# Kernel tuning notes

Hardware: AMD Instinct MI355X
Metric: run time of the kernel (lower is better)

The kernel has to match this reference:

```python
import jax, jax.numpy as jnp
import numpy as np

B, T, V, RNN, N_OBJ = 1024, 48, 2000, 64, 25

def _lstm_cell(x, h, c, W_ih, W_hh, b_ih, b_hh):
    # PyTorch LSTMCell: gate order i, f, g, o
    gates = x @ W_ih.T + h @ W_hh.T + b_ih + b_hh
    i, f, g, o = jnp.split(gates, 4, axis=-1)
    c2 = jax.nn.sigmoid(f) * c + jax.nn.sigmoid(i) * jnp.tanh(g)
    return jax.nn.sigmoid(o) * jnp.tanh(c2), c2

def _attend(memory, h2, w1, b1, w2, b2):
    # memory: [B, 25, 4], h2: [B, 25, RNN]
    x = jnp.concatenate([h2, memory], axis=2)            # [B, 25, RNN+4]
    s = (jax.nn.relu(x @ w1.T + b1) @ w2.T + b2)[..., 0]  # [B, 25]
    w = jax.nn.softmax(s, axis=1)
    return jnp.einsum('bn,bnd->bd', w, memory)            # [B, 4]

def setup_inputs() -> dict:
    key = jax.random.key(0)
    ks = jax.random.split(key, 32)
    f = lambda k, shape: jax.random.normal(k, shape, dtype=jnp.float32) * 0.05
    return dict(
        inst=jax.random.randint(ks[0], (B, T), 1, V + 1),
        prev_canvas=jax.random.uniform(ks[1], (B, N_OBJ, 4), dtype=jnp.float32),
        final_canvas=jax.random.uniform(ks[2], (B, N_OBJ, 4), dtype=jnp.float32),
        embed=f(ks[3], (V + 1, 64)),
        W_ih_att=f(ks[4], (4 * RNN, 128)), W_hh_att=f(ks[5], (4 * RNN, RNN)),
        b_ih_att=f(ks[6], (4 * RNN,)), b_hh_att=f(ks[7], (4 * RNN,)),
        W_ih_lang=f(ks[8], (4 * RNN, 2 * RNN)), W_hh_lang=f(ks[9], (4 * RNN, RNN)),
        b_ih_lang=f(ks[10], (4 * RNN,)), b_hh_lang=f(ks[11], (4 * RNN,)),
        fc_out_w=f(ks[12], (V + 1, RNN)), fc_out_b=f(ks[13], (V + 1,)),
        att1_w1=f(ks[14], (32, RNN + 4)), att1_b1=f(ks[15], (32,)),
        att1_w2=f(ks[16], (1, 32)), att1_b2=f(ks[17], (1,)),
        att2_w1=f(ks[18], (32, RNN + 4)), att2_b1=f(ks[19], (32,)),
        att2_w2=f(ks[20], (1, 32)), att2_b2=f(ks[21], (1,)),
        trans_w1=f(ks[22], (32, 8)), trans_b1=f(ks[23], (32,)),
        trans_w2=f(ks[24], (RNN, 32)), trans_b2=f(ks[25], (RNN,)),
    )

def reference(inst, prev_canvas, final_canvas, embed, W_ih_att, W_hh_att, b_ih_att, b_hh_att, W_ih_lang, W_hh_lang, b_ih_lang, b_hh_lang, fc_out_w, fc_out_b, att1_w1, att1_b1, att1_w2, att1_b2, att2_w1, att2_b1, att2_w2, att2_b2, trans_w1, trans_b1, trans_w2, trans_b2):
    # compute_diff_canvas
    mask = prev_canvas.sum(axis=2, keepdims=True) > 0
    diff_canvas = jnp.where(mask, -1.0, final_canvas)  # [B, 25, 4]
    batch = inst.shape[0]
    h0 = jnp.zeros((batch, RNN), dtype=jnp.float32)

    def step(carry, it):
        h_att, c_att, h_lang, c_lang = carry
        xt = embed[it]  # [B, 64]
        h_att, c_att = _lstm_cell(jnp.concatenate([h_lang, xt], axis=1), h_att, c_att, W_ih_att, W_hh_att, b_ih_att, b_hh_att)
        h2 = jnp.broadcast_to(h_att[:, None, :], (batch, N_OBJ, RNN))
        a1 = _attend(diff_canvas, h2, att1_w1, att1_b1, att1_w2, att1_b2)
        a2 = _attend(prev_canvas, h2, att2_w1, att2_b1, att2_w2, att2_b2)
        att = jnp.concatenate([a1, a2], axis=1)  # [B, 8]
        att = jax.nn.relu(att @ trans_w1.T + trans_b1) @ trans_w2.T + trans_b2  # [B, RNN]
        h_lang, c_lang = _lstm_cell(jnp.concatenate([att, h_att], axis=1), h_lang, c_lang, W_ih_lang, W_hh_lang, b_ih_lang, b_hh_lang)
        logp = jax.nn.log_softmax(h_lang @ fc_out_w.T + fc_out_b, axis=1)  # [B, V+1]
        return (h_att, c_att, h_lang, c_lang), logp

    xs = inst[:, :-1].T  # [T-1, B]; inst has no all-zero column so all steps run
    _, outs = jax.lax.scan(step, (h0, h0, h0, h0), xs)
    return jnp.transpose(outs, (1, 0, 2))  # [B, T-1, V+1]
```

## Files before the change

kernel.cpp:

```cpp
#include <hip/hip_runtime.h>

#define BATCH 1024
#define TT 48
#define NSTEP 47
#define VOC 2001
#define RNN 64
#define NOBJ 25
#define NROWS (BATCH*NSTEP)
#define NTILE 126
#define NPAD 2016

typedef _Float16 h2 __attribute__((ext_vector_type(2)));
typedef _Float16 h8 __attribute__((ext_vector_type(8)));
typedef short short8 __attribute__((ext_vector_type(8)));
typedef float f32x4 __attribute__((ext_vector_type(4)));

__device__ __forceinline__ float fdot2f(h2 a, h2 b, float c){
#if __has_builtin(__builtin_amdgcn_fdot2)
    return __builtin_amdgcn_fdot2(a, b, c, false);
#else
    return c + (float)a[0]*(float)b[0] + (float)a[1]*(float)b[1];
#endif
}

__device__ __forceinline__ float dot8(h8 w, h8 x, float acc){
    acc = fdot2f(__builtin_shufflevector(w,w,0,1), __builtin_shufflevector(x,x,0,1), acc);
    acc = fdot2f(__builtin_shufflevector(w,w,2,3), __builtin_shufflevector(x,x,2,3), acc);
    acc = fdot2f(__builtin_shufflevector(w,w,4,5), __builtin_shufflevector(x,x,4,5), acc);
    acc = fdot2f(__builtin_shufflevector(w,w,6,7), __builtin_shufflevector(x,x,6,7), acc);
    return acc;
}

__device__ __forceinline__ float sigf(float x){ return 1.f/(1.f+__expf(-x)); }
__device__ __forceinline__ float tanh_(float x){
    float e = __expf(2.f*fminf(x, 15.f));
    return (e-1.f)/(e+1.f);
}
__device__ __forceinline__ unsigned short bf16r(float f){
    unsigned u = __float_as_uint(f);
    return (unsigned short)((u + 0x7FFFu + ((u>>16)&1u)) >> 16);
}


__global__ void k_pre(const float* __restrict__ prev, const float* __restrict__ fin,
                      const float* __restrict__ a1w1, const float* __restrict__ a1b1,
                      const float* __restrict__ a2w1, const float* __restrict__ a2b1,
                      float* __restrict__ diff, float* __restrict__ pre1, float* __restrict__ pre2){
    int idx = blockIdx.x*256 + threadIdx.x;
    if (idx >= BATCH*NOBJ) return;
    float p0 = prev[idx*4+0], p1 = prev[idx*4+1], p2 = prev[idx*4+2], p3 = prev[idx*4+3];
    bool masked = (p0+p1+p2+p3) > 0.f;
    float d0 = masked ? -1.f : fin[idx*4+0];
    float d1 = masked ? -1.f : fin[idx*4+1];
    float d2 = masked ? -1.f : fin[idx*4+2];
    float d3 = masked ? -1.f : fin[idx*4+3];
    diff[idx*4+0]=d0; diff[idx*4+1]=d1; diff[idx*4+2]=d2; diff[idx*4+3]=d3;
    for (int j=0;j<32;++j){
        const float* w1 = a1w1 + j*68 + 64;
        const float* w2 = a2w1 + j*68 + 64;
        pre1[idx*32+j] = a1b1[j] + d0*w1[0] + d1*w1[1] + d2*w1[2] + d3*w1[3];
        pre2[idx*32+j] = a2b1[j] + p0*w2[0] + p1*w2[1] + p2*w2[2] + p3*w2[3];
    }
}

__global__ void k_embw(const float* __restrict__ embed, const float* __restrict__ Wia,
                       const float* __restrict__ bia, const float* __restrict__ bha,
                       float* __restrict__ embW){
    int v = blockIdx.x, g = threadIdx.x;
    __shared__ float er[64];
    if (g < 64) er[g] = embed[v*64+g];
    __syncthreads();
    float acc = bia[g] + bha[g];
    const float* wr = Wia + g*128 + 64;
    #pragma unroll 8
    for (int k=0;k<64;++k) acc += er[k]*wr[k];
    embW[v*256+g] = acc;
}

__global__ void k_packrow(const float* __restrict__ src, _Float16* __restrict__ dst,
                          int srcK, int koff, int K, int total){
    int idx = blockIdx.x*256 + threadIdx.x;
    if (idx >= total) return;
    int k = idx % K, g = idx / K;
    dst[idx] = (_Float16)src[g*srcK + koff + k];
}

__global__ void k_weff(const float* __restrict__ Wil, const float* __restrict__ tw2,
                       const float* __restrict__ tb2, const float* __restrict__ bil,
                       const float* __restrict__ bhl, _Float16* __restrict__ Weff,
                       float* __restrict__ biasL2){
    __shared__ float t2[64*32];
    int g = threadIdx.x;
    for (int i=g;i<2048;i+=256) t2[i] = tw2[i];
    __syncthreads();
    float accs[32];
    #pragma unroll
    for (int m=0;m<32;++m) accs[m]=0.f;
    float bf = bil[g] + bhl[g];
    for (int d=0;d<64;++d){
        float w = Wil[g*128 + d];
        bf += w * tb2[d];
        #pragma unroll
        for (int m=0;m<32;++m) accs[m] += w * t2[d*32+m];
    }
    #pragma unroll
    for (int m=0;m<32;++m) Weff[g*32+m] = (_Float16)accs[m];
    biasL2[g] = bf;
}

__global__ void k_fcbpad(const float* __restrict__ fcb_in, float* __restrict__ fcb){
    int i = blockIdx.x*256 + threadIdx.x;
    if (i >= NPAD) return;
    fcb[i] = (i < VOC) ? fcb_in[i] : -1e30f;
}

__global__ void k_fragb(const float* __restrict__ fcw, unsigned short* __restrict__ fragB){
    int idx = blockIdx.x*256 + threadIdx.x;
    int lane = idx & 63, kh = (idx>>6)&1, tile = idx>>7;
    int n = tile*16 + (lane & 15);
    int k = kh*32 + (lane >> 4)*8;
    unsigned short* d = fragB + (size_t)((tile*2+kh)*64 + lane)*8;
    #pragma unroll
    for (int i=0;i<8;++i)
        d[i] = (n < VOC) ? bf16r(fcw[n*64 + k + i]) : (unsigned short)0;
}


__global__ __launch_bounds__(256, 2) void k_recur(
    const int* __restrict__ inst, const float* __restrict__ embW,
    const float* __restrict__ diff, const float* __restrict__ prev,
    const float* __restrict__ pre1, const float* __restrict__ pre2,
    const _Float16* __restrict__ attLp, const _Float16* __restrict__ attHp,
    const _Float16* __restrict__ wLhap, const _Float16* __restrict__ wLhlp,
    const _Float16* __restrict__ Weffp, const float* __restrict__ biasL2,
    const _Float16* __restrict__ w1fp,
    const float* __restrict__ a1w2, const float* __restrict__ a1b2,
    const float* __restrict__ a2w2, const float* __restrict__ a2b2,
    const float* __restrict__ tw1, const float* __restrict__ tb1,
    unsigned short* __restrict__ h_hist)
{
    const int tid = threadIdx.x;
    const int rb  = blockIdx.x;

    __shared__ float gbuf[256];
    __shared__ __align__(16) _Float16 hl16[64];
    __shared__ __align__(16) _Float16 ha16[64];
    __shared__ __align__(16) _Float16 u16[32];
    __shared__ float hpart[64];
    __shared__ float sbuf[2][32];
    __shared__ float att8s[8];
    __shared__ __align__(16) float preS[2][25][36];
    __shared__ float memS[2*25*4];
    __shared__ __align__(16) _Float16 w1fS[64*72];
    __shared__ float tw1S[256], tb1S[32], w2S[2][32], b2S[2];
    __shared__ int   tokS[NSTEP];
    __shared__ float biasS[256];

    for (int i=tid;i<NSTEP;i+=256) tokS[i] = inst[rb*TT + i];
    for (int i=tid;i<1600;i+=256){
        int h = i/800, rem = i - h*800, n = rem>>5, k = rem&31;
        preS[h][n][k] = (h ? pre2 : pre1)[(size_t)(rb*NOBJ+n)*32 + k];
    }
    for (int i=tid;i<200;i+=256)
        memS[i] = (i<100 ? diff : prev)[(size_t)rb*100 + (i%100)];
    for (int i=tid;i<4096;i+=256){
        int r = i>>6, k = i&63;
        w1fS[r*72+k] = w1fp[i];
    }
    if (tid<256) tw1S[tid] = tw1[tid];
    if (tid<32)  tb1S[tid] = tb1[tid];
    if (tid<64)  w2S[tid>>5][tid&31] = (tid<32 ? a1w2 : a2w2)[tid&31];
    if (tid<2)   b2S[tid] = tid ? a2b2[0] : a1b2[0];
    biasS[tid] = biasL2[tid];
    if (tid<64){ hl16[tid]=(_Float16)0.f; ha16[tid]=(_Float16)0.f; }

    h8 wAL[8], wAH[8], wLHa[8], wLHl[8], wEf[4];
    {
        const h8* p0 = (const h8*)(attLp + (size_t)tid*64);
        const h8* p1 = (const h8*)(attHp + (size_t)tid*64);
        const h8* p2 = (const h8*)(wLhap + (size_t)tid*64);
        const h8* p3 = (const h8*)(wLhlp + (size_t)tid*64);
        const h8* p4 = (const h8*)(Weffp + (size_t)tid*32);
        #pragma unroll
        for (int k=0;k<8;++k){ wAL[k]=p0[k]; wAH[k]=p1[k]; wLHa[k]=p2[k]; wLHl[k]=p3[k]; }
        #pragma unroll
        for (int k=0;k<4;++k) wEf[k]=p4[k];
    }
    float c_att = 0.f, c_lang = 0.f;
    __syncthreads();

    const int wave = tid>>6, lane = tid&63;

    for (int t=0;t<NSTEP;++t){
        float acc = embW[(size_t)tokS[t]*256 + tid];
        {
            const h8* xh = (const h8*)hl16;
            const h8* xa = (const h8*)ha16;
            #pragma unroll
            for (int k=0;k<8;++k) acc = dot8(wAL[k], xh[k], acc);
            #pragma unroll
            for (int k=0;k<8;++k) acc = dot8(wAH[k], xa[k], acc);
        }
        gbuf[tid] = acc;
        __syncthreads();
        if (tid < 64){
            float i_=sigf(gbuf[tid]), f_=sigf(gbuf[64+tid]);
            float g_=tanh_(gbuf[128+tid]), o_=sigf(gbuf[192+tid]);
            c_att = f_*c_att + i_*g_;
            ha16[tid] = (_Float16)(o_*tanh_(c_att));
        }
        __syncthreads();

        if (wave==1){
            const h8* xa = (const h8*)ha16;
            const h8* wr = (const h8*)&w1fS[lane*72];
            float hp = 0.f;
            #pragma unroll
            for (int k=0;k<8;++k) hp = dot8(wr[k], xa[k], hp);
            hpart[lane] = hp;
        }
        __syncthreads();

        if (wave==2){
            int half = lane>>5, n = lane&31;
            if (n < NOBJ){
                const float4* pp = (const float4*)&preS[half][n][0];
                const float*  hp = &hpart[half*32];
                const float*  w2 = &w2S[half][0];
                float a = b2S[half];
                #pragma unroll
                for (int i=0;i<8;++i){
                    float4 pv = pp[i];
                    a += fmaxf(hp[4*i+0]+pv.x,0.f)*w2[4*i+0]
                       + fmaxf(hp[4*i+1]+pv.y,0.f)*w2[4*i+1]
                       + fmaxf(hp[4*i+2]+pv.z,0.f)*w2[4*i+2]
                       + fmaxf(hp[4*i+3]+pv.w,0.f)*w2[4*i+3];
                }
                sbuf[half][n] = a;
            }
        }
        __syncthreads();

        if (tid>=192 && tid<200){
            int j = tid-192, half = j>>2, d = j&3;
            const float* ss = &sbuf[half][0];
            const float* mem = &memS[half*100];
            float m = -1e30f;
            for (int n=0;n<NOBJ;++n) m = fmaxf(m, ss[n]);
            float s=0.f, a=0.f;
            for (int n=0;n<NOBJ;++n){ float e=__expf(ss[n]-m); s+=e; a+=e*mem[n*4+d]; }
            att8s[j] = a/s;
        }
        __syncthreads();

        if (tid < 32){
            float u = tb1S[tid];
            #pragma unroll
            for (int i=0;i<8;++i) u += att8s[i]*tw1S[tid*8+i];
            u16[tid] = (_Float16)fmaxf(u, 0.f);
        }
        __syncthreads();

        float acc2 = biasS[tid];
        {
            const h8* xu = (const h8*)u16;
            const h8* xa = (const h8*)ha16;
            const h8* xh = (const h8*)hl16;
            #pragma unroll
            for (int k=0;k<4;++k) acc2 = dot8(wEf[k], xu[k], acc2);
            #pragma unroll
            for (int k=0;k<8;++k) acc2 = dot8(wLHa[k], xa[k], acc2);
            #pragma unroll
            for (int k=0;k<8;++k) acc2 = dot8(wLHl[k], xh[k], acc2);
        }
        gbuf[tid] = acc2;
        __syncthreads();
        if (tid < 64){
            float i_=sigf(gbuf[tid]), f_=sigf(gbuf[64+tid]);
            float g_=tanh_(gbuf[128+tid]), o_=sigf(gbuf[192+tid]);
            c_lang = f_*c_lang + i_*g_;
            float hL = o_*tanh_(c_lang);
            hl16[tid] = (_Float16)hL;
            h_hist[((size_t)rb*NSTEP + t)*64 + tid] = bf16r(hL);
        }
        __syncthreads();
    }
}


__global__ __launch_bounds__(256) void k_fc(const unsigned short* __restrict__ h_hist,
                                            const unsigned short* __restrict__ fragB,
                                            const float* __restrict__ fcb,
                                            float* __restrict__ out)
{
    const int tid = threadIdx.x;
    const int w = tid >> 6, lane = tid & 63;
    const int q = lane >> 4, l16 = lane & 15;
    const int rowbase = blockIdx.x*16;

    const short8 a0 = *(const short8*)(h_hist + (size_t)(rowbase + l16)*64 + q*8);
    const short8 a1 = *(const short8*)(h_hist + (size_t)(rowbase + l16)*64 + 32 + q*8);

    float m[4], s[4];
    #pragma unroll
    for (int i=0;i<4;++i){ m[i] = -INFINITY; s[i] = 0.f; }

    for (int tile = w; tile < NTILE; tile += 4){
        const short8 b0 = *(const short8*)(fragB + (size_t)((tile*2+0)*64 + lane)*8);
        const short8 b1 = *(const short8*)(fragB + (size_t)((tile*2+1)*64 + lane)*8);
        f32x4 acc = {0.f,0.f,0.f,0.f};
        acc = __builtin_amdgcn_mfma_f32_16x16x32_bf16(a0, b0, acc, 0, 0, 0);
        acc = __builtin_amdgcn_mfma_f32_16x16x32_bf16(a1, b1, acc, 0, 0, 0);
        float bias = fcb[tile*16 + l16];
        #pragma unroll
        for (int i=0;i<4;++i){
            float v = acc[i] + bias;
            float nm = fmaxf(m[i], v);
            s[i] = s[i]*__expf(m[i]-nm) + __expf(v-nm);
            m[i] = nm;
        }
    }
    #pragma unroll
    for (int i=0;i<4;++i){
        #pragma unroll
        for (int off=1; off<16; off<<=1){
            float om = __shfl_xor(m[i], off, 64);
            float os = __shfl_xor(s[i], off, 64);
            float nm = fmaxf(m[i], om);
            s[i] = s[i]*__expf(m[i]-nm) + os*__expf(om-nm);
            m[i] = nm;
        }
    }
    __shared__ float lm[4][16], ls[4][16], fm[16], fl[16];
    if (l16 == 0){
        #pragma unroll
        for (int i=0;i<4;++i){ lm[w][q*4+i] = m[i]; ls[w][q*4+i] = s[i]; }
    }
    __syncthreads();
    if (tid < 16){
        float M = -INFINITY, S = 0.f;
        #pragma unroll
        for (int ww=0;ww<4;++ww){
            float om = lm[ww][tid], os = ls[ww][tid];
            float nm = fmaxf(M, om);
            S = S*__expf(M-nm) + os*__expf(om-nm);
            M = nm;
        }
        fm[tid] = M; fl[tid] = __logf(S);
    }
    __syncthreads();
    float Mr[4], Lr[4];
    #pragma unroll
    for (int i=0;i<4;++i){ Mr[i] = fm[q*4+i]; Lr[i] = fl[q*4+i]; }

    for (int tile = w; tile < NTILE; tile += 4){
        const short8 b0 = *(const short8*)(fragB + (size_t)((tile*2+0)*64 + lane)*8);
        const short8 b1 = *(const short8*)(fragB + (size_t)((tile*2+1)*64 + lane)*8);
        f32x4 acc = {0.f,0.f,0.f,0.f};
        acc = __builtin_amdgcn_mfma_f32_16x16x32_bf16(a0, b0, acc, 0, 0, 0);
        acc = __builtin_amdgcn_mfma_f32_16x16x32_bf16(a1, b1, acc, 0, 0, 0);
        int col = tile*16 + l16;
        if (col < VOC){
            float bias = fcb[col];
            #pragma unroll
            for (int i=0;i<4;++i)
                out[(size_t)(rowbase + q*4 + i)*VOC + col] = acc[i] + bias - Mr[i] - Lr[i];
        }
    }
}


extern "C" void kernel_launch(void* const* d_in, const int* in_sizes, int n_in,
                              void* d_out, int out_size, void* d_ws, size_t ws_size,
                              hipStream_t stream)
{
    const int*   inst  = (const int*)  d_in[0];
    const float* prev  = (const float*)d_in[1];
    const float* fin   = (const float*)d_in[2];
    const float* embed = (const float*)d_in[3];
    const float* Wia   = (const float*)d_in[4];
    const float* Wha   = (const float*)d_in[5];
    const float* bia   = (const float*)d_in[6];
    const float* bha   = (const float*)d_in[7];
    const float* Wil   = (const float*)d_in[8];
    const float* Whl   = (const float*)d_in[9];
    const float* bil   = (const float*)d_in[10];
    const float* bhl   = (const float*)d_in[11];
    const float* fcw   = (const float*)d_in[12];
    const float* fcbi  = (const float*)d_in[13];
    const float* a1w1  = (const float*)d_in[14];
    const float* a1b1  = (const float*)d_in[15];
    const float* a1w2  = (const float*)d_in[16];
    const float* a1b2  = (const float*)d_in[17];
    const float* a2w1  = (const float*)d_in[18];
    const float* a2b1  = (const float*)d_in[19];
    const float* a2w2  = (const float*)d_in[20];
    const float* a2b2  = (const float*)d_in[21];
    const float* tw1   = (const float*)d_in[22];
    const float* tb1   = (const float*)d_in[23];
    const float* tw2   = (const float*)d_in[24];
    const float* tb2   = (const float*)d_in[25];
    float* out = (float*)d_out;

    char* wsb = (char*)d_ws; size_t off = 0;
    auto alloc = [&](size_t bytes)->char*{
        char* p = wsb + off; off = (off + bytes + 511) & ~(size_t)511; return p;
    };
    float*          embW  = (float*)alloc((size_t)VOC*256*4);
    float*          diff  = (float*)alloc((size_t)BATCH*NOBJ*4*4);
    float*          pre1  = (float*)alloc((size_t)BATCH*NOBJ*32*4);
    float*          pre2  = (float*)alloc((size_t)BATCH*NOBJ*32*4);
    _Float16*       attLp = (_Float16*)alloc((size_t)256*64*2);
    _Float16*       attHp = (_Float16*)alloc((size_t)256*64*2);
    _Float16*       wLhap = (_Float16*)alloc((size_t)256*64*2);
    _Float16*       wLhlp = (_Float16*)alloc((size_t)256*64*2);
    _Float16*       Weffp = (_Float16*)alloc((size_t)256*32*2);
    _Float16*       w1fp  = (_Float16*)alloc((size_t)64*64*2);
    float*          biasL2= (float*)alloc(256*4);
    float*          fcb   = (float*)alloc((size_t)NPAD*4);
    unsigned short* hhist = (unsigned short*)alloc((size_t)NROWS*64*2);
    unsigned short* fragB = (unsigned short*)alloc((size_t)NTILE*2*64*8*2);

    k_pre    <<<(BATCH*NOBJ+255)/256, 256, 0, stream>>>(prev, fin, a1w1, a1b1, a2w1, a2b1, diff, pre1, pre2);
    k_embw   <<<VOC, 256, 0, stream>>>(embed, Wia, bia, bha, embW);
    k_packrow<<<64, 256, 0, stream>>>(Wia, attLp, 128, 0,  64, 256*64);
    k_packrow<<<64, 256, 0, stream>>>(Wha, attHp,  64, 0,  64, 256*64);
    k_packrow<<<64, 256, 0, stream>>>(Wil, wLhap, 128, 64, 64, 256*64);
    k_packrow<<<64, 256, 0, stream>>>(Whl, wLhlp,  64, 0,  64, 256*64);
    k_packrow<<<8,  256, 0, stream>>>(a1w1, w1fp,       68, 0, 64, 32*64);
    k_packrow<<<8,  256, 0, stream>>>(a2w1, w1fp+32*64, 68, 0, 64, 32*64);
    k_weff   <<<1, 256, 0, stream>>>(Wil, tw2, tb2, bil, bhl, Weffp, biasL2);
    k_fcbpad <<<(NPAD+255)/256, 256, 0, stream>>>(fcbi, fcb);
    k_fragb  <<<63, 256, 0, stream>>>(fcw, fragB);

    k_recur<<<BATCH, 256, 0, stream>>>(inst, embW, diff, prev, pre1, pre2,
                                       attLp, attHp, wLhap, wLhlp, Weffp, biasL2, w1fp,
                                       a1w2, a1b2, a2w2, a2b2, tw1, tb1, hhist);

    k_fc<<<NROWS/16, 256, 0, stream>>>(hhist, fragB, fcb, out);
}
```

Baseline: 863.7 us.

## Process two batch rows per recurrent block and collapse attention phases into fewer barriers

Each k_recur block now handles two batch rows, so each thread's register-resident LSTM weights are reused for two dot products and half as many blocks are launched. The attention, softmax and transform stages are merged into one wave-local section, with waves 0 and 1 each owning one row, which cuts the per-step barriers from eight to four. The h_lang recurrent term is folded into the first phase, the next step's embedding is prefetched, and plain syncthreads is replaced by an LDS-wait plus s_barrier. The trade-offs are fewer blocks in flight (512) to hide latency, more register pressure, and relying on intra-wave ordering of LDS writes and reads within the merged section.

```diff
diff --git a/kernel.cpp b/kernel.cpp
--- a/kernel.cpp
+++ b/kernel.cpp
@@ -39,6 +39,12 @@
 __device__ __forceinline__ unsigned short bf16r(float f){
     unsigned u = __float_as_uint(f);
     return (unsigned short)((u + 0x7FFFu + ((u>>16)&1u)) >> 16);
+}
+
+__device__ __forceinline__ void block_sync_lds(){
+    asm volatile("s_waitcnt lgkmcnt(0)" ::: "memory");
+    __builtin_amdgcn_s_barrier();
+    asm volatile("" ::: "memory");
 }
 
 
@@ -125,7 +131,6 @@
         d[i] = (n < VOC) ? bf16r(fcw[n*64 + k + i]) : (unsigned short)0;
 }
 
-
 __global__ __launch_bounds__(256, 2) void k_recur(
     const int* __restrict__ inst, const float* __restrict__ embW,
     const float* __restrict__ diff, const float* __restrict__ prev,
@@ -140,39 +145,40 @@
     unsigned short* __restrict__ h_hist)
 {
     const int tid = threadIdx.x;
-    const int rb  = blockIdx.x;
-
-    __shared__ float gbuf[256];
-    __shared__ __align__(16) _Float16 hl16[64];
-    __shared__ __align__(16) _Float16 ha16[64];
-    __shared__ __align__(16) _Float16 u16[32];
-    __shared__ float hpart[64];
-    __shared__ float sbuf[2][32];
-    __shared__ float att8s[8];
-    __shared__ __align__(16) float preS[2][25][36];
-    __shared__ float memS[2*25*4];
+    const int rb0 = blockIdx.x*2;
+
+    __shared__ float gbuf[2][256];
+    __shared__ __align__(16) _Float16 hl16[2][64];
+    __shared__ __align__(16) _Float16 ha16[2][64];
+    __shared__ __align__(16) _Float16 u16v[2][32];
+    __shared__ float hpart[2][64];
+    __shared__ float sbuf[2][2][32];
+    __shared__ float att8s[2][8];
+    __shared__ __align__(16) float preS[2][2][25][36];
+    __shared__ float memS[2][200];
     __shared__ __align__(16) _Float16 w1fS[64*72];
-    __shared__ float tw1S[256], tb1S[32], w2S[2][32], b2S[2];
-    __shared__ int   tokS[NSTEP];
-    __shared__ float biasS[256];
-
-    for (int i=tid;i<NSTEP;i+=256) tokS[i] = inst[rb*TT + i];
-    for (int i=tid;i<1600;i+=256){
-        int h = i/800, rem = i - h*800, n = rem>>5, k = rem&31;
-        preS[h][n][k] = (h ? pre2 : pre1)[(size_t)(rb*NOBJ+n)*32 + k];
-    }
-    for (int i=tid;i<200;i+=256)
-        memS[i] = (i<100 ? diff : prev)[(size_t)rb*100 + (i%100)];
+    __shared__ float tw1T[256];
+    __shared__ float w2S[2][32];
+    __shared__ float b2S[2];
+    __shared__ int   tokS[2][NSTEP];
+
+    for (int i=tid;i<2*NSTEP;i+=256){ int r=i/NSTEP, s=i-r*NSTEP; tokS[r][s]=inst[(rb0+r)*TT+s]; }
+    for (int i=tid;i<3200;i+=256){
+        int r = i/1600, rem = i - r*1600, h = rem/800, rem2 = rem - h*800, n = rem2>>5, k = rem2&31;
+        preS[r][h][n][k] = (h ? pre2 : pre1)[(size_t)((rb0+r)*NOBJ+n)*32 + k];
+    }
+    for (int i=tid;i<400;i+=256){
+        int r = i/200, rem = i - r*200;
+        memS[r][rem] = (rem<100 ? diff : prev)[(size_t)(rb0+r)*100 + (rem%100)];
+    }
     for (int i=tid;i<4096;i+=256){
-        int r = i>>6, k = i&63;
-        w1fS[r*72+k] = w1fp[i];
-    }
-    if (tid<256) tw1S[tid] = tw1[tid];
-    if (tid<32)  tb1S[tid] = tb1[tid];
-    if (tid<64)  w2S[tid>>5][tid&31] = (tid<32 ? a1w2 : a2w2)[tid&31];
-    if (tid<2)   b2S[tid] = tid ? a2b2[0] : a1b2[0];
-    biasS[tid] = biasL2[tid];
-    if (tid<64){ hl16[tid]=(_Float16)0.f; ha16[tid]=(_Float16)0.f; }
+        int rw = i>>6, k = i&63;
+        w1fS[rw*72+k] = w1fp[i];
+    }
+    { int m = tid&31, k = tid>>5; tw1T[k*32+m] = tw1[m*8+k]; }
+    if (tid<64) w2S[tid>>5][tid&31] = (tid<32 ? a1w2 : a2w2)[tid&31];
+    if (tid<2)  b2S[tid] = tid ? a2b2[0] : a1b2[0];
+    for (int i=tid;i<128;i+=256){ hl16[i>>6][i&63]=(_Float16)0.f; ha16[i>>6][i&63]=(_Float16)0.f; }
 
     h8 wAL[8], wAH[8], wLHa[8], wLHl[8], wEf[4];
     {
@@ -186,104 +192,121 @@
         #pragma unroll
         for (int k=0;k<4;++k) wEf[k]=p4[k];
     }
+    const float biasv = biasL2[tid];
+    const float tb1v  = ((tid&63) < 32) ? tb1[tid&63] : 0.f;
     float c_att = 0.f, c_lang = 0.f;
     __syncthreads();
 
     const int wave = tid>>6, lane = tid&63;
 
+    const h8* xh0 = (const h8*)&hl16[0][0];
+    const h8* xh1 = (const h8*)&hl16[1][0];
+    const h8* xa0 = (const h8*)&ha16[0][0];
+    const h8* xa1 = (const h8*)&ha16[1][0];
+    const h8* xu0 = (const h8*)&u16v[0][0];
+    const h8* xu1 = (const h8*)&u16v[1][0];
+
+    float ew0 = embW[(size_t)tokS[0][0]*256 + tid];
+    float ew1 = embW[(size_t)tokS[1][0]*256 + tid];
+
+    #pragma unroll 1
     for (int t=0;t<NSTEP;++t){
-        float acc = embW[(size_t)tokS[t]*256 + tid];
+        float a0 = ew0, a1 = ew1, p0 = biasv, p1 = biasv;
         {
-            const h8* xh = (const h8*)hl16;
-            const h8* xa = (const h8*)ha16;
-            #pragma unroll
-            for (int k=0;k<8;++k) acc = dot8(wAL[k], xh[k], acc);
-            #pragma unroll
-            for (int k=0;k<8;++k) acc = dot8(wAH[k], xa[k], acc);
-        }
-        gbuf[tid] = acc;
-        __syncthreads();
-        if (tid < 64){
-            float i_=sigf(gbuf[tid]), f_=sigf(gbuf[64+tid]);
-            float g_=tanh_(gbuf[128+tid]), o_=sigf(gbuf[192+tid]);
+            int tn = (t+1 < NSTEP) ? t+1 : NSTEP-1;
+            ew0 = embW[(size_t)tokS[0][tn]*256 + tid];
+            ew1 = embW[(size_t)tokS[1][tn]*256 + tid];
+        }
+        #pragma unroll
+        for (int k=0;k<8;++k){
+            h8 h0 = xh0[k], h1 = xh1[k];
+            a0 = dot8(wAL[k],  h0, a0);  a1 = dot8(wAL[k],  h1, a1);
+            p0 = dot8(wLHl[k], h0, p0);  p1 = dot8(wLHl[k], h1, p1);
+        }
+        #pragma unroll
+        for (int k=0;k<8;++k){
+            h8 v0 = xa0[k], v1 = xa1[k];
+            a0 = dot8(wAH[k], v0, a0);   a1 = dot8(wAH[k], v1, a1);
+        }
+        gbuf[0][tid] = a0; gbuf[1][tid] = a1;
+        block_sync_lds();
+
+        if (wave < 2){
+            const int r = wave;
+            float gi = gbuf[r][lane], gf = gbuf[r][64+lane];
+            float gg = gbuf[r][128+lane], go = gbuf[r][192+lane];
+            float i_=sigf(gi), f_=sigf(gf), g_=tanh_(gg), o_=sigf(go);
             c_att = f_*c_att + i_*g_;
-            ha16[tid] = (_Float16)(o_*tanh_(c_att));
-        }
-        __syncthreads();
-
-        if (wave==1){
-            const h8* xa = (const h8*)ha16;
-            const h8* wr = (const h8*)&w1fS[lane*72];
-            float hp = 0.f;
-            #pragma unroll
-            for (int k=0;k<8;++k) hp = dot8(wr[k], xa[k], hp);
-            hpart[lane] = hp;
-        }
-        __syncthreads();
-
-        if (wave==2){
-            int half = lane>>5, n = lane&31;
-            if (n < NOBJ){
-                const float4* pp = (const float4*)&preS[half][n][0];
-                const float*  hp = &hpart[half*32];
-                const float*  w2 = &w2S[half][0];
-                float a = b2S[half];
+            ha16[r][lane] = (_Float16)(o_*tanh_(c_att));
+            {
+                const h8* xa = (const h8*)&ha16[r][0];
+                const h8* wr = (const h8*)&w1fS[lane*72];
+                float hp = 0.f;
                 #pragma unroll
-                for (int i=0;i<8;++i){
-                    float4 pv = pp[i];
-                    a += fmaxf(hp[4*i+0]+pv.x,0.f)*w2[4*i+0]
-                       + fmaxf(hp[4*i+1]+pv.y,0.f)*w2[4*i+1]
-                       + fmaxf(hp[4*i+2]+pv.z,0.f)*w2[4*i+2]
-                       + fmaxf(hp[4*i+3]+pv.w,0.f)*w2[4*i+3];
+                for (int k=0;k<8;++k) hp = dot8(wr[k], xa[k], hp);
+                hpart[r][lane] = hp;
+            }
+            {
+                int half = lane>>5, n = lane&31;
+                if (n < NOBJ){
+                    const float4* pp = (const float4*)&preS[r][half][n][0];
+                    const float*  hp = &hpart[r][half*32];
+                    const float*  w2 = &w2S[half][0];
+                    float a = b2S[half];
+                    #pragma unroll
+                    for (int i=0;i<8;++i){
+                        float4 pv = pp[i];
+                        a += fmaxf(hp[4*i+0]+pv.x,0.f)*w2[4*i+0]
+                           + fmaxf(hp[4*i+1]+pv.y,0.f)*w2[4*i+1]
+                           + fmaxf(hp[4*i+2]+pv.z,0.f)*w2[4*i+2]
+                           + fmaxf(hp[4*i+3]+pv.w,0.f)*w2[4*i+3];
+                    }
+                    sbuf[r][half][n] = a;
                 }
-                sbuf[half][n] = a;
             }
-        }
-        __syncthreads();
-
-        if (tid>=192 && tid<200){
-            int j = tid-192, half = j>>2, d = j&3;
-            const float* ss = &sbuf[half][0];
-            const float* mem = &memS[half*100];
-            float m = -1e30f;
-            for (int n=0;n<NOBJ;++n) m = fmaxf(m, ss[n]);
-            float s=0.f, a=0.f;
-            for (int n=0;n<NOBJ;++n){ float e=__expf(ss[n]-m); s+=e; a+=e*mem[n*4+d]; }
-            att8s[j] = a/s;
-        }
-        __syncthreads();
-
-        if (tid < 32){
-            float u = tb1S[tid];
-            #pragma unroll
-            for (int i=0;i<8;++i) u += att8s[i]*tw1S[tid*8+i];
-            u16[tid] = (_Float16)fmaxf(u, 0.f);
-        }
-        __syncthreads();
-
-        float acc2 = biasS[tid];
-        {
-            const h8* xu = (const h8*)u16;
-            const h8* xa = (const h8*)ha16;
-            const h8* xh = (const h8*)hl16;
-            #pragma unroll
-            for (int k=0;k<4;++k) acc2 = dot8(wEf[k], xu[k], acc2);
-            #pragma unroll
-            for (int k=0;k<8;++k) acc2 = dot8(wLHa[k], xa[k], acc2);
-            #pragma unroll
-            for (int k=0;k<8;++k) acc2 = dot8(wLHl[k], xh[k], acc2);
-        }
-        gbuf[tid] = acc2;
-        __syncthreads();
-        if (tid < 64){
-            float i_=sigf(gbuf[tid]), f_=sigf(gbuf[64+tid]);
-            float g_=tanh_(gbuf[128+tid]), o_=sigf(gbuf[192+tid]);
+            if (lane < 8){
+                int half = lane>>2, d = lane&3;
+                const float* ss  = &sbuf[r][half][0];
+                const float* mem = &memS[r][half*100];
+                float m = -1e30f;
+                for (int n=0;n<NOBJ;++n) m = fmaxf(m, ss[n]);
+                float s=0.f, a=0.f;
+                for (int n=0;n<NOBJ;++n){ float e=__expf(ss[n]-m); s+=e; a+=e*mem[n*4+d]; }
+                att8s[r][lane] = a/s;
+            }
+            if (lane < 32){
+                float u = tb1v;
+                #pragma unroll
+                for (int i=0;i<8;++i) u += att8s[r][i]*tw1T[i*32+lane];
+                u16v[r][lane] = (_Float16)fmaxf(u, 0.f);
+            }
+        }
+        block_sync_lds();
+
+        #pragma unroll
+        for (int k=0;k<4;++k){
+            h8 u0 = xu0[k], u1 = xu1[k];
+            p0 = dot8(wEf[k], u0, p0);   p1 = dot8(wEf[k], u1, p1);
+        }
+        #pragma unroll
+        for (int k=0;k<8;++k){
+            h8 v0 = xa0[k], v1 = xa1[k];
+            p0 = dot8(wLHa[k], v0, p0);  p1 = dot8(wLHa[k], v1, p1);
+        }
+        gbuf[0][tid] = p0; gbuf[1][tid] = p1;
+        block_sync_lds();
+
+        if (wave < 2){
+            const int r = wave;
+            float gi = gbuf[r][lane], gf = gbuf[r][64+lane];
+            float gg = gbuf[r][128+lane], go = gbuf[r][192+lane];
+            float i_=sigf(gi), f_=sigf(gf), g_=tanh_(gg), o_=sigf(go);
             c_lang = f_*c_lang + i_*g_;
             float hL = o_*tanh_(c_lang);
-            hl16[tid] = (_Float16)hL;
-            h_hist[((size_t)rb*NSTEP + t)*64 + tid] = bf16r(hL);
-        }
-        __syncthreads();
+            hl16[r][lane] = (_Float16)hL;
+            h_hist[((size_t)(rb0+r)*NSTEP + t)*64 + lane] = bf16r(hL);
+        }
+        block_sync_lds();
     }
 }
 
@@ -433,9 +456,9 @@
     k_fcbpad <<<(NPAD+255)/256, 256, 0, stream>>>(fcbi, fcb);
     k_fragb  <<<63, 256, 0, stream>>>(fcw, fragB);
 
-    k_recur<<<BATCH, 256, 0, stream>>>(inst, embW, diff, prev, pre1, pre2,
-                                       attLp, attHp, wLhap, wLhlp, Weffp, biasL2, w1fp,
-                                       a1w2, a1b2, a2w2, a2b2, tw1, tb1, hhist);
+    k_recur<<<BATCH/2, 256, 0, stream>>>(inst, embW, diff, prev, pre1, pre2,
+                                         attLp, attHp, wLhap, wLhlp, Weffp, biasL2, w1fp,
+                                         a1w2, a1b2, a2w2, a2b2, tw1, tb1, hhist);
 
     k_fc<<<NROWS/16, 256, 0, stream>>>(hhist, fragB, fcb, out);
 }
```

New measurement: 828.8 us. 1.04x faster.
